# Optimization experiments

Hardware: AMD Instinct MI355X
Metric: run time of the kernel (lower is better)

## Reference

```python
import jax, jax.numpy as jnp
import numpy as np

C = 256      # in/out channels
PSI = 4
W = C // PSI          # window width = 64
D = W // 2            # stride = 32
HEADS = 2 * PSI - 1   # 7


def conv_bn_relu(x, Wmat, scale, bias):
    # 1x1 conv (no bias) + inference-mode BN (folded to per-channel scale/bias) + ReLU
    y = jnp.einsum('oc,bcn->bon', Wmat, x)
    return jax.nn.relu(y * scale[:, None] + bias[:, None])


def setup_inputs() -> dict:
    key = jax.random.key(0)
    ks = jax.random.split(key, 16)
    B, N = 4, 2048
    x = jax.random.normal(ks[0], (B, C, N), dtype=jnp.float32)
    Wq = jax.random.normal(ks[1], (C, C), dtype=jnp.float32) / np.sqrt(C)
    Wk = jax.random.normal(ks[2], (C, C), dtype=jnp.float32) / np.sqrt(C)
    Wv = jax.random.normal(ks[3], (C, C), dtype=jnp.float32) / np.sqrt(C)
    sq = jax.random.uniform(ks[4], (C,), dtype=jnp.float32, minval=0.5, maxval=1.5)
    bq = jax.random.normal(ks[5], (C,), dtype=jnp.float32) * 0.1
    sk = jax.random.uniform(ks[6], (C,), dtype=jnp.float32, minval=0.5, maxval=1.5)
    bk = jax.random.normal(ks[7], (C,), dtype=jnp.float32) * 0.1
    sv = jax.random.uniform(ks[8], (C,), dtype=jnp.float32, minval=0.5, maxval=1.5)
    bv = jax.random.normal(ks[9], (C,), dtype=jnp.float32) * 0.1
    Wf = jax.random.normal(ks[10], (C, HEADS * W), dtype=jnp.float32) / np.sqrt(HEADS * W)
    bf = jax.random.normal(ks[11], (C,), dtype=jnp.float32) * 0.1
    sf = jax.random.uniform(ks[12], (C,), dtype=jnp.float32, minval=0.5, maxval=1.5)
    bff = jax.random.normal(ks[13], (C,), dtype=jnp.float32) * 0.1
    return dict(x=x, Wq=Wq, sq=sq, bq=bq, Wk=Wk, sk=sk, bk=bk,
                Wv=Wv, sv=sv, bv=bv, Wf=Wf, bf=bf, sf=sf, bff=bff)


def reference(x, Wq, sq, bq, Wk, sk, bk, Wv, sv, bv, Wf, bf, sf, bff):
    q = conv_bn_relu(x, Wq, sq, bq)   # [B, C, N]
    k = conv_bn_relu(x, Wk, sk, bk)
    v = conv_bn_relu(x, Wv, sv, bv)

    # overlapping channel windows: head m covers channels [m*D, m*D+W)
    win = jnp.arange(HEADS)[:, None] * D + jnp.arange(W)[None, :]  # [HEADS, W]
    qw = q[:, win, :]  # [B, HEADS, W, N]
    kw = k[:, win, :]
    vw = v[:, win, :]

    # a_m = q_m^T k_m over channel window -> [B, HEADS, N, N]
    attn = jnp.einsum('bhwn,bhwm->bhnm', qw, kw)
    attn = jax.nn.softmax(attn, axis=-1)
    # o_m = (a_m v_m^T)^T -> [B, HEADS, W, N]
    o = jnp.einsum('bhnm,bhwm->bhwn', attn, vw)

    B, _, _, N = o.shape
    O = o.reshape(B, HEADS * W, N)  # concat heads along channel dim

    # fusion: 1x1 conv (with bias) + BN + ReLU
    y = jnp.einsum('oc,bcn->bon', Wf, O) + bf[:, None]
    return jax.nn.relu(y * sf[:, None] + bff[:, None])
```

## Files before the change

kernel.cpp:

```cpp
#include <hip/hip_runtime.h>
#include <hip/hip_bf16.h>

typedef __attribute__((ext_vector_type(8))) short bf16x8;
typedef __attribute__((ext_vector_type(4))) float f32x4;

namespace {
constexpr int kC = 256;
constexpr int kN = 2048;
constexpr int kB = 4;
constexpr int kHeads = 7;
constexpr int kOC = kHeads * 64;
constexpr float kLog2e = 1.44269504f;
}

static __device__ __forceinline__ float bf2f(ushort u) {
    union { unsigned u; float f; } v; v.u = ((unsigned)u) << 16;
    return v.f;
}
static __device__ __forceinline__ unsigned pk_bf16(float a, float b) {
    __hip_bfloat162 h = __float22bfloat162_rn(make_float2(a, b));
    union { __hip_bfloat162 h; unsigned u; } v; v.h = h;
    return v.u;
}
static __device__ __forceinline__ ushort4 pack4bf(float a, float b, float c, float d) {
    union { ushort4 s; uint2 u; } v;
    v.u.x = pk_bf16(a, b); v.u.y = pk_bf16(c, d);
    return v.s;
}
static __device__ __forceinline__ float fexp2(float x) {
#if __has_builtin(__builtin_amdgcn_exp2f)
    return __builtin_amdgcn_exp2f(x);
#else
    return exp2f(x);
#endif
}
static __device__ __forceinline__ void g2l16(const ushort* g, ushort* l) {
    __builtin_amdgcn_global_load_lds(
        (const __attribute__((address_space(1))) void*)g,
        (__attribute__((address_space(3))) void*)l,
        16, 0, 0);
}

__global__ __launch_bounds__(256) void prep_kernel(
    const float* __restrict__ x,
    const float* __restrict__ Wq, const float* __restrict__ Wk,
    const float* __restrict__ Wv, const float* __restrict__ Wf,
    ushort* __restrict__ xT,
    ushort* __restrict__ wq, ushort* __restrict__ wk,
    ushort* __restrict__ wv, ushort* __restrict__ wf)
{
    __shared__ float T[64][65];
    const int bid = blockIdx.x;
    const int tid = threadIdx.x;
    if (bid < 512) {
        const int nt = bid & 31, ct = (bid >> 5) & 3, b = bid >> 7;
        const float* xb = x + ((size_t)b * kC + ct * 64) * kN + nt * 64;
#pragma unroll
        for (int p = 0; p < 16; ++p) {
            int idx = p * 256 + tid;
            int cc = idx >> 6, nn = idx & 63;
            T[cc][nn] = xb[(size_t)cc * kN + nn];
        }
        __syncthreads();
        ushort* xTb = xT + ((size_t)b * kN + nt * 64) * kC + ct * 64;
#pragma unroll
        for (int p = 0; p < 4; ++p) {
            int nn = p * 16 + (tid >> 4);
            int c4 = (tid & 15) * 4;
            *(ushort4*)&xTb[(size_t)nn * kC + c4] =
                pack4bf(T[c4 + 0][nn], T[c4 + 1][nn], T[c4 + 2][nn], T[c4 + 3][nn]);
        }
    } else {
        const int j = bid - 512;
        const int which = j / 112, bx = j % 112;
        const float* src = which == 0 ? Wq : which == 1 ? Wk : which == 2 ? Wv : Wf;
        ushort* dst      = which == 0 ? wq : which == 1 ? wk : which == 2 ? wv : wf;
        int n = (which == 3) ? kC * kOC : kC * kC;
        int i = (bx * 256 + tid) * 4;
        if (i < n) {
            float4 v = *(const float4*)(src + i);
            *(ushort4*)(dst + i) = pack4bf(v.x, v.y, v.z, v.w);
        }
    }
}

__global__ __launch_bounds__(256, 2) void qkv_kernel(
    const ushort* __restrict__ xT,
    const ushort* __restrict__ Wqb, const ushort* __restrict__ Wkb, const ushort* __restrict__ Wvb,
    const float* __restrict__ sq, const float* __restrict__ bq,
    const float* __restrict__ sk, const float* __restrict__ bk,
    const float* __restrict__ sv, const float* __restrict__ bv,
    ushort* __restrict__ qT, ushort* __restrict__ kT, ushort* __restrict__ vB)
{
    const int nt  = blockIdx.x;
    const int ot  = blockIdx.y;
    const int b   = blockIdx.z / 3;
    const int mat = blockIdx.z % 3;
    const ushort* Wb = mat == 0 ? Wqb : mat == 1 ? Wkb : Wvb;
    const float* sm = mat == 0 ? sq : mat == 1 ? sk : sv;
    const float* bm = mat == 0 ? bq : mat == 1 ? bk : bv;

    __shared__ __align__(16) ushort lds[4][128 * 64];

    const int tid = threadIdx.x;
    const int lane = tid & 63, wav = tid >> 6;
    const int quad = lane >> 4, l16 = lane & 15;

    const ushort* xTb = xT + ((size_t)b * kN + nt * 128) * kC;
    const ushort* Wt  = Wb + (size_t)(ot * 128) * kC;

    f32x4 acc[8][2];
#pragma unroll
    for (int mt = 0; mt < 8; ++mt)
#pragma unroll
        for (int ntt = 0; ntt < 2; ++ntt)
#pragma unroll
            for (int r = 0; r < 4; ++r) acc[mt][ntt][r] = 0.f;

    const int sa   = lane >> 3;
    const int sblk = (lane & 7) ^ sa;
    auto dmaK = [&](int k0, int buf) {
#pragma unroll
        for (int p = 0; p < 4; ++p) {
            int row = wav * 32 + p * 8 + sa;
            size_t so = (size_t)row * kC + k0 + sblk * 8;
            int dbase = (wav * 32 + p * 8) * 64;
            g2l16(Wt + so,  &lds[buf][dbase]);
            g2l16(xTb + so, &lds[2 + buf][dbase]);
        }
    };

    dmaK(0, 0);
    __syncthreads();

    for (int kt = 0; kt < 4; ++kt) {
        const int cur = kt & 1;
        const bool more = (kt < 3);
        if (more) dmaK((kt + 1) * 64, cur ^ 1);

        const ushort* rowB = (mat < 2) ? lds[cur] : lds[2 + cur];
        const ushort* colB = (mat < 2) ? lds[2 + cur] : lds[cur];
#pragma unroll
        for (int ks = 0; ks < 2; ++ks) {
            bf16x8 bfr[2];
#pragma unroll
            for (int ntt = 0; ntt < 2; ++ntt) {
                int row = wav * 32 + ntt * 16 + l16;
                bfr[ntt] = *(const bf16x8*)&colB[row * 64 + (((ks * 4 + quad) ^ (row & 7)) * 8)];
            }
#pragma unroll
            for (int mt = 0; mt < 8; ++mt) {
                int row = mt * 16 + l16;
                bf16x8 af = *(const bf16x8*)&rowB[row * 64 + (((ks * 4 + quad) ^ (row & 7)) * 8)];
#pragma unroll
                for (int ntt = 0; ntt < 2; ++ntt)
                    acc[mt][ntt] = __builtin_amdgcn_mfma_f32_16x16x32_bf16(
                        af, bfr[ntt], acc[mt][ntt], 0, 0, 0);
            }
        }
        __syncthreads();
    }

    ushort* sT = &lds[0][0];
    const float qs = (mat == 0) ? kLog2e : 1.f;

    if (mat < 2) {
#pragma unroll
        for (int mt = 0; mt < 8; ++mt) {
            float4 sc4 = *(const float4*)&sm[ot * 128 + mt * 16 + quad * 4];
            float4 bi4 = *(const float4*)&bm[ot * 128 + mt * 16 + quad * 4];
#pragma unroll
            for (int ntt = 0; ntt < 2; ++ntt) {
                int nrow = wav * 32 + ntt * 16 + l16;
                float v0 = fmaf(acc[mt][ntt][0], sc4.x, bi4.x) * qs;
                float v1 = fmaf(acc[mt][ntt][1], sc4.y, bi4.y) * qs;
                float v2 = fmaf(acc[mt][ntt][2], sc4.z, bi4.z) * qs;
                float v3 = fmaf(acc[mt][ntt][3], sc4.w, bi4.w) * qs;
                int cb = (mt * 2 + (quad >> 1)) ^ (nrow & 15);
                *(ushort4*)&sT[nrow * 128 + cb * 8 + (quad & 1) * 4] =
                    pack4bf(v0 > 0.f ? v0 : 0.f, v1 > 0.f ? v1 : 0.f,
                            v2 > 0.f ? v2 : 0.f, v3 > 0.f ? v3 : 0.f);
            }
        }
        __syncthreads();
        ushort* out = (mat == 0) ? qT : kT;
#pragma unroll
        for (int p = 0; p < 8; ++p) {
            int idx = p * 256 + tid;
            int row = idx >> 4, blk = idx & 15;
            int4 d = *(const int4*)&sT[row * 128 + ((blk ^ (row & 15)) * 8)];
            *(int4*)&out[((size_t)b * kN + nt * 128 + row) * kC + ot * 128 + blk * 8] = d;
        }
    } else {
#pragma unroll
        for (int ntt = 0; ntt < 2; ++ntt) {
            int orow = wav * 32 + ntt * 16 + l16;
            float sc = sm[ot * 128 + orow], bi = bm[ot * 128 + orow];
#pragma unroll
            for (int mt = 0; mt < 8; ++mt) {
                float v0 = fmaf(acc[mt][ntt][0], sc, bi);
                float v1 = fmaf(acc[mt][ntt][1], sc, bi);
                float v2 = fmaf(acc[mt][ntt][2], sc, bi);
                float v3 = fmaf(acc[mt][ntt][3], sc, bi);
                int cb = (mt * 2 + (quad >> 1)) ^ (orow & 15);
                *(ushort4*)&sT[orow * 128 + cb * 8 + (quad & 1) * 4] =
                    pack4bf(v0 > 0.f ? v0 : 0.f, v1 > 0.f ? v1 : 0.f,
                            v2 > 0.f ? v2 : 0.f, v3 > 0.f ? v3 : 0.f);
            }
        }
        __syncthreads();
#pragma unroll
        for (int p = 0; p < 8; ++p) {
            int idx = p * 256 + tid;
            int row = idx >> 4, blk = idx & 15;
            int4 d = *(const int4*)&sT[row * 128 + ((blk ^ (row & 15)) * 8)];
            *(int4*)&vB[((size_t)b * kC + ot * 128 + row) * kN + nt * 128 + blk * 8] = d;
        }
    }
}

__global__ __launch_bounds__(512, 2) void attn_kernel(
    const ushort* __restrict__ qT, const ushort* __restrict__ kT,
    const ushort* __restrict__ vB,
    ushort* __restrict__ Opart)
{
    const int j   = blockIdx.x;
    const int lid = (j & 7) * 28 + (j >> 3);
    const int b   = lid / 56;
    const int r2  = lid % 56;
    const int h   = r2 % 7;
    const int nt  = r2 / 7;
    const int n0  = nt * 256;

    const int tid = threadIdx.x;
    const int lane = tid & 63, wav = tid >> 6;
    const int quad = lane >> 4, l16 = lane & 15;

    __shared__ __align__(16) ushort sKV[2][8192];

    const ushort* qTb = qT + (size_t)b * kN * kC;
    const ushort* kTb = kT + (size_t)b * kN * kC;
    const ushort* vbb = vB + ((size_t)b * kC + h * 32) * kN;

    const int arr   = wav >> 2;
    const int rbase = (wav & 3) * 16;

    bf16x8 qf[2][2];
#pragma unroll
    for (int kk = 0; kk < 2; ++kk)
#pragma unroll
        for (int nt2 = 0; nt2 < 2; ++nt2) {
            int ng = n0 + wav * 32 + nt2 * 16 + l16;
            qf[kk][nt2] = *(const bf16x8*)(qTb + (size_t)ng * kC + h * 32 + kk * 32 + quad * 8);
        }

    f32x4 oacc[4][2];
#pragma unroll
    for (int wt = 0; wt < 4; ++wt)
#pragma unroll
        for (int nt2 = 0; nt2 < 2; ++nt2)
#pragma unroll
            for (int r = 0; r < 4; ++r) oacc[wt][nt2][r] = 0.f;
    float li[2] = {0.f, 0.f};

    const int NIT = kN / 64;

    const int sa   = lane >> 3;
    const int sblk = (lane & 7) ^ sa;
    auto dmaTile = [&](int m0, int buf) {
#pragma unroll
        for (int p = 0; p < 2; ++p) {
            int rl = rbase + p * 8 + sa;
            const ushort* src = (arr == 0)
                ? (kTb + (size_t)(m0 + rl) * kC + h * 32 + sblk * 8)
                : (vbb + (size_t)rl * kN + m0 + sblk * 8);
            g2l16(src, &sKV[buf][arr * 4096 + (rbase + p * 8) * 64]);
        }
    };

    dmaTile(0, 0);
    __syncthreads();

    for (int it = 0; it < NIT; ++it) {
        const int cur = it & 1;
        const bool more = (it + 1 < NIT);
        if (more) dmaTile((it + 1) * 64, cur ^ 1);

        const ushort* sK = &sKV[cur][0];
        const ushort* sV = &sKV[cur][4096];

        f32x4 sacc[4][2];
#pragma unroll
        for (int mt = 0; mt < 4; ++mt)
#pragma unroll
            for (int nt2 = 0; nt2 < 2; ++nt2)
#pragma unroll
                for (int r = 0; r < 4; ++r) sacc[mt][nt2][r] = 0.f;
        __builtin_amdgcn_s_setprio(1);
#pragma unroll
        for (int kk = 0; kk < 2; ++kk)
#pragma unroll
            for (int mt = 0; mt < 4; ++mt) {
                int row = mt * 16 + l16;
                bf16x8 af = *(const bf16x8*)&sK[row * 64 + (((kk * 4 + quad) ^ (row & 7)) * 8)];
#pragma unroll
                for (int nt2 = 0; nt2 < 2; ++nt2)
                    sacc[mt][nt2] = __builtin_amdgcn_mfma_f32_16x16x32_bf16(
                        af, qf[kk][nt2], sacc[mt][nt2], 0, 0, 0);
            }
        __builtin_amdgcn_s_setprio(0);

        unsigned d[2][4][2];
#pragma unroll
        for (int nt2 = 0; nt2 < 2; ++nt2) {
            float sum = 0.f;
#pragma unroll
            for (int mt = 0; mt < 4; ++mt) {
                float p0 = fexp2(sacc[mt][nt2][0]);
                float p1 = fexp2(sacc[mt][nt2][1]);
                float p2 = fexp2(sacc[mt][nt2][2]);
                float p3 = fexp2(sacc[mt][nt2][3]);
                sum += (p0 + p1) + (p2 + p3);
                d[nt2][mt][0] = pk_bf16(p0, p1);
                d[nt2][mt][1] = pk_bf16(p2, p3);
            }
            li[nt2] += sum;
        }

#pragma unroll
        for (int ks = 0; ks < 2; ++ks) {
            bf16x8 pf[2];
#pragma unroll
            for (int nt2 = 0; nt2 < 2; ++nt2) {
                union { unsigned w[4]; bf16x8 v8; } pu;
#if __has_builtin(__builtin_amdgcn_permlane32_swap) && __has_builtin(__builtin_amdgcn_permlane16_swap)
#pragma unroll
                for (int rd = 0; rd < 2; ++rd) {
                    unsigned a = d[nt2][2 * ks][rd], bb = d[nt2][2 * ks + 1][rd];
                    auto r32 = __builtin_amdgcn_permlane32_swap(a, bb, false, false);
                    auto r16 = __builtin_amdgcn_permlane16_swap(r32[0], r32[1], false, false);
                    pu.w[rd]     = r16[0];
                    pu.w[2 + rd] = r16[1];
                }
#else
                const int gx = ((lane & 16) << 1) + l16;
                const int gy = gx + 16;
                const bool lo = (lane < 32);
#pragma unroll
                for (int rd = 0; rd < 2; ++rd) {
                    unsigned u = d[nt2][2 * ks][rd], v = d[nt2][2 * ks + 1][rd];
                    unsigned xu = (unsigned)__shfl((int)u, gx);
                    unsigned xv = (unsigned)__shfl((int)v, gx);
                    unsigned yu = (unsigned)__shfl((int)u, gy);
                    unsigned yv = (unsigned)__shfl((int)v, gy);
                    pu.w[rd]     = lo ? xu : xv;
                    pu.w[2 + rd] = lo ? yu : yv;
                }
#endif
                pf[nt2] = pu.v8;
            }
            __builtin_amdgcn_s_setprio(1);
#pragma unroll
            for (int wt = 0; wt < 4; ++wt) {
                int wr = wt * 16 + l16;
                bf16x8 vf = *(const bf16x8*)&sV[wr * 64 + (((ks * 4 + quad) ^ (wr & 7)) * 8)];
#pragma unroll
                for (int nt2 = 0; nt2 < 2; ++nt2)
                    oacc[wt][nt2] = __builtin_amdgcn_mfma_f32_16x16x32_bf16(
                        vf, pf[nt2], oacc[wt][nt2], 0, 0, 0);
            }
            __builtin_amdgcn_s_setprio(0);
        }

        __syncthreads();
    }

#pragma unroll
    for (int nt2 = 0; nt2 < 2; ++nt2) {
        li[nt2] += __shfl_xor(li[nt2], 16);
        li[nt2] += __shfl_xor(li[nt2], 32);
    }
    ushort* sT = &sKV[0][0];
#pragma unroll
    for (int wt = 0; wt < 4; ++wt)
#pragma unroll
        for (int nt2 = 0; nt2 < 2; ++nt2) {
            float inv = 1.f / li[nt2];
            int nrow = wav * 32 + nt2 * 16 + l16;
            int cb = (wt * 2 + (quad >> 1)) ^ (nrow & 7);
            *(ushort4*)&sT[nrow * 64 + cb * 8 + (quad & 1) * 4] =
                pack4bf(oacc[wt][nt2][0] * inv, oacc[wt][nt2][1] * inv,
                        oacc[wt][nt2][2] * inv, oacc[wt][nt2][3] * inv);
        }
    __syncthreads();
    int rsub = tid >> 3, blk = tid & 7;
#pragma unroll
    for (int p = 0; p < 4; ++p) {
        int row = p * 64 + rsub;
        int4 dd = *(const int4*)&sT[row * 64 + ((blk ^ (row & 7)) * 8)];
        *(int4*)&Opart[((size_t)b * kN + n0 + row) * kOC + h * 64 + blk * 8] = dd;
    }
}

__global__ __launch_bounds__(256, 4) void proj_kernel(
    const ushort* __restrict__ Opart, const ushort* __restrict__ Wfb,
    const float* __restrict__ bf_, const float* __restrict__ sf,
    const float* __restrict__ bff, float* __restrict__ out)
{
    const int nt = blockIdx.x;
    const int ot = blockIdx.y;
    const int b  = blockIdx.z;
    __shared__ __align__(16) ushort sA[2][64 * 64];
    __shared__ __align__(16) ushort sB[2][64 * 64];
    const int tid = threadIdx.x;
    const int lane = tid & 63, wav = tid >> 6;
    const int quad = lane >> 4, l16 = lane & 15;

    const ushort* Wt = Wfb + (size_t)(ot * 64) * kOC;
    const ushort* Ob = Opart + ((size_t)b * kN + nt * 64) * kOC;

    f32x4 acc[4];
#pragma unroll
    for (int ntt = 0; ntt < 4; ++ntt)
#pragma unroll
        for (int r = 0; r < 4; ++r) acc[ntt][r] = 0.f;

    const int sa   = lane >> 3;
    const int sblk = (lane & 7) ^ sa;
    auto dmaT = [&](int kt, int buf) {
        int k0 = kt * 64;
#pragma unroll
        for (int p = 0; p < 2; ++p) {
            int row = wav * 16 + p * 8 + sa;
            int dbase = (wav * 16 + p * 8) * 64;
            g2l16(Wt + (size_t)row * kOC + k0 + sblk * 8, &sA[buf][dbase]);
            g2l16(Ob + (size_t)row * kOC + k0 + sblk * 8, &sB[buf][dbase]);
        }
    };

    dmaT(0, 0);
    __syncthreads();

    for (int kt = 0; kt < 7; ++kt) {
        const int cur = kt & 1;
        const bool more = (kt < 6);
        if (more) dmaT(kt + 1, cur ^ 1);
#pragma unroll
        for (int ks = 0; ks < 2; ++ks) {
            int arow = wav * 16 + l16;
            bf16x8 af = *(const bf16x8*)&sA[cur][arow * 64 + (((ks * 4 + quad) ^ (arow & 7)) * 8)];
#pragma unroll
            for (int ntt = 0; ntt < 4; ++ntt) {
                int brow = ntt * 16 + l16;
                bf16x8 bfr = *(const bf16x8*)&sB[cur][brow * 64 + (((ks * 4 + quad) ^ (brow & 7)) * 8)];
                acc[ntt] = __builtin_amdgcn_mfma_f32_16x16x32_bf16(af, bfr, acc[ntt], 0, 0, 0);
            }
        }
        __syncthreads();
    }
#pragma unroll
    for (int r = 0; r < 4; ++r) {
        int o = ot * 64 + wav * 16 + quad * 4 + r;
        float bfv = bf_[o], sfv = sf[o], bffv = bff[o];
#pragma unroll
        for (int ntt = 0; ntt < 4; ++ntt) {
            int n = nt * 64 + ntt * 16 + l16;
            float y = fmaf(acc[ntt][r] + bfv, sfv, bffv);
            out[((size_t)b * kC + o) * kN + n] = y > 0.f ? y : 0.f;
        }
    }
}

extern "C" void kernel_launch(void* const* d_in, const int* in_sizes, int n_in,
                              void* d_out, int out_size, void* d_ws, size_t ws_size,
                              hipStream_t stream) {
    const float* x   = (const float*)d_in[0];
    const float* Wq  = (const float*)d_in[1];
    const float* sq  = (const float*)d_in[2];
    const float* bq  = (const float*)d_in[3];
    const float* Wk  = (const float*)d_in[4];
    const float* sk  = (const float*)d_in[5];
    const float* bk  = (const float*)d_in[6];
    const float* Wv  = (const float*)d_in[7];
    const float* sv  = (const float*)d_in[8];
    const float* bv  = (const float*)d_in[9];
    const float* Wf  = (const float*)d_in[10];
    const float* bf_ = (const float*)d_in[11];
    const float* sf  = (const float*)d_in[12];
    const float* bff = (const float*)d_in[13];
    float* out = (float*)d_out;

    char* ws = (char*)d_ws;
    ushort* xT  = (ushort*)(ws);
    ushort* Wqb = (ushort*)(ws + 4194304);
    ushort* Wkb = (ushort*)(ws + 4325376);
    ushort* Wvb = (ushort*)(ws + 4456448);
    ushort* Wfb = (ushort*)(ws + 4587520);
    ushort* qT  = (ushort*)(ws + 4816896);
    ushort* kT  = (ushort*)(ws + 9011200);
    ushort* vB  = (ushort*)(ws + 13205504);
    ushort* Opart = (ushort*)(ws + 17399808);

    prep_kernel<<<dim3(960), 256, 0, stream>>>(
        x, Wq, Wk, Wv, Wf, xT, Wqb, Wkb, Wvb, Wfb);
    qkv_kernel<<<dim3(kN / 128, kC / 128, kB * 3), 256, 0, stream>>>(
        xT, Wqb, Wkb, Wvb, sq, bq, sk, bk, sv, bv, qT, kT, vB);
    attn_kernel<<<dim3(224), 512, 0, stream>>>(
        qT, kT, vB, Opart);
    proj_kernel<<<dim3(kN / 64, kC / 64, kB), 256, 0, stream>>>(
        Opart, Wfb, bf_, sf, bff, out);
}
```

Baseline: 153.2 us.

## Split QKV GEMM tile across 8 waves and remap blocks across XCDs

The QKV projection kernel now runs 512 threads per block instead of 256. Each wave computes a 64x32 sub-tile instead of 128x32, halving per-wave accumulators and adding latency hiding. The 3D grid is flattened to 384 blocks with a remapping that groups consecutive logical tiles onto the same XCD, intended to improve L2 reuse of x and weights. The extra waves share the same LDS buffers and barriers, so synchronisation cost per block rises.

```diff
diff --git a/kernel.cpp b/kernel.cpp
--- a/kernel.cpp
+++ b/kernel.cpp
@@ -84,7 +84,7 @@
     }
 }
 
-__global__ __launch_bounds__(256, 2) void qkv_kernel(
+__global__ __launch_bounds__(512, 2) void qkv_kernel(
     const ushort* __restrict__ xT,
     const ushort* __restrict__ Wqb, const ushort* __restrict__ Wkb, const ushort* __restrict__ Wvb,
     const float* __restrict__ sq, const float* __restrict__ bq,
@@ -92,10 +92,13 @@
     const float* __restrict__ sv, const float* __restrict__ bv,
     ushort* __restrict__ qT, ushort* __restrict__ kT, ushort* __restrict__ vB)
 {
-    const int nt  = blockIdx.x;
-    const int ot  = blockIdx.y;
-    const int b   = blockIdx.z / 3;
-    const int mat = blockIdx.z % 3;
+    const int j   = blockIdx.x;
+    const int lid = (j & 7) * 48 + (j >> 3);
+    const int nt  = lid & 15;
+    const int ot  = (lid >> 4) & 1;
+    const int zz  = lid >> 5;
+    const int b   = zz / 3;
+    const int mat = zz % 3;
     const ushort* Wb = mat == 0 ? Wqb : mat == 1 ? Wkb : Wvb;
     const float* sm = mat == 0 ? sq : mat == 1 ? sk : sv;
     const float* bm = mat == 0 ? bq : mat == 1 ? bk : bv;
@@ -105,13 +108,15 @@
     const int tid = threadIdx.x;
     const int lane = tid & 63, wav = tid >> 6;
     const int quad = lane >> 4, l16 = lane & 15;
+    const int oh = wav >> 2;
+    const int nq = wav & 3;
 
     const ushort* xTb = xT + ((size_t)b * kN + nt * 128) * kC;
     const ushort* Wt  = Wb + (size_t)(ot * 128) * kC;
 
-    f32x4 acc[8][2];
-#pragma unroll
-    for (int mt = 0; mt < 8; ++mt)
+    f32x4 acc[4][2];
+#pragma unroll
+    for (int mt = 0; mt < 4; ++mt)
 #pragma unroll
         for (int ntt = 0; ntt < 2; ++ntt)
 #pragma unroll
@@ -121,10 +126,10 @@
     const int sblk = (lane & 7) ^ sa;
     auto dmaK = [&](int k0, int buf) {
 #pragma unroll
-        for (int p = 0; p < 4; ++p) {
-            int row = wav * 32 + p * 8 + sa;
+        for (int p = 0; p < 2; ++p) {
+            int row = wav * 16 + p * 8 + sa;
             size_t so = (size_t)row * kC + k0 + sblk * 8;
-            int dbase = (wav * 32 + p * 8) * 64;
+            int dbase = (wav * 16 + p * 8) * 64;
             g2l16(Wt + so,  &lds[buf][dbase]);
             g2l16(xTb + so, &lds[2 + buf][dbase]);
         }
@@ -145,12 +150,12 @@
             bf16x8 bfr[2];
 #pragma unroll
             for (int ntt = 0; ntt < 2; ++ntt) {
-                int row = wav * 32 + ntt * 16 + l16;
+                int row = nq * 32 + ntt * 16 + l16;
                 bfr[ntt] = *(const bf16x8*)&colB[row * 64 + (((ks * 4 + quad) ^ (row & 7)) * 8)];
             }
 #pragma unroll
-            for (int mt = 0; mt < 8; ++mt) {
-                int row = mt * 16 + l16;
+            for (int mt = 0; mt < 4; ++mt) {
+                int row = oh * 64 + mt * 16 + l16;
                 bf16x8 af = *(const bf16x8*)&rowB[row * 64 + (((ks * 4 + quad) ^ (row & 7)) * 8)];
 #pragma unroll
                 for (int ntt = 0; ntt < 2; ++ntt)
@@ -166,17 +171,17 @@
 
     if (mat < 2) {
 #pragma unroll
-        for (int mt = 0; mt < 8; ++mt) {
-            float4 sc4 = *(const float4*)&sm[ot * 128 + mt * 16 + quad * 4];
-            float4 bi4 = *(const float4*)&bm[ot * 128 + mt * 16 + quad * 4];
+        for (int mt = 0; mt < 4; ++mt) {
+            float4 sc4 = *(const float4*)&sm[ot * 128 + oh * 64 + mt * 16 + quad * 4];
+            float4 bi4 = *(const float4*)&bm[ot * 128 + oh * 64 + mt * 16 + quad * 4];
 #pragma unroll
             for (int ntt = 0; ntt < 2; ++ntt) {
-                int nrow = wav * 32 + ntt * 16 + l16;
+                int nrow = nq * 32 + ntt * 16 + l16;
                 float v0 = fmaf(acc[mt][ntt][0], sc4.x, bi4.x) * qs;
                 float v1 = fmaf(acc[mt][ntt][1], sc4.y, bi4.y) * qs;
                 float v2 = fmaf(acc[mt][ntt][2], sc4.z, bi4.z) * qs;
                 float v3 = fmaf(acc[mt][ntt][3], sc4.w, bi4.w) * qs;
-                int cb = (mt * 2 + (quad >> 1)) ^ (nrow & 15);
+                int cb = (oh * 8 + mt * 2 + (quad >> 1)) ^ (nrow & 15);
                 *(ushort4*)&sT[nrow * 128 + cb * 8 + (quad & 1) * 4] =
                     pack4bf(v0 > 0.f ? v0 : 0.f, v1 > 0.f ? v1 : 0.f,
                             v2 > 0.f ? v2 : 0.f, v3 > 0.f ? v3 : 0.f);
@@ -185,8 +190,8 @@
         __syncthreads();
         ushort* out = (mat == 0) ? qT : kT;
 #pragma unroll
-        for (int p = 0; p < 8; ++p) {
-            int idx = p * 256 + tid;
+        for (int p = 0; p < 4; ++p) {
+            int idx = p * 512 + tid;
             int row = idx >> 4, blk = idx & 15;
             int4 d = *(const int4*)&sT[row * 128 + ((blk ^ (row & 15)) * 8)];
             *(int4*)&out[((size_t)b * kN + nt * 128 + row) * kC + ot * 128 + blk * 8] = d;
@@ -194,15 +199,15 @@
     } else {
 #pragma unroll
         for (int ntt = 0; ntt < 2; ++ntt) {
-            int orow = wav * 32 + ntt * 16 + l16;
+            int orow = nq * 32 + ntt * 16 + l16;
             float sc = sm[ot * 128 + orow], bi = bm[ot * 128 + orow];
 #pragma unroll
-            for (int mt = 0; mt < 8; ++mt) {
+            for (int mt = 0; mt < 4; ++mt) {
                 float v0 = fmaf(acc[mt][ntt][0], sc, bi);
                 float v1 = fmaf(acc[mt][ntt][1], sc, bi);
                 float v2 = fmaf(acc[mt][ntt][2], sc, bi);
                 float v3 = fmaf(acc[mt][ntt][3], sc, bi);
-                int cb = (mt * 2 + (quad >> 1)) ^ (orow & 15);
+                int cb = (oh * 8 + mt * 2 + (quad >> 1)) ^ (orow & 15);
                 *(ushort4*)&sT[orow * 128 + cb * 8 + (quad & 1) * 4] =
                     pack4bf(v0 > 0.f ? v0 : 0.f, v1 > 0.f ? v1 : 0.f,
                             v2 > 0.f ? v2 : 0.f, v3 > 0.f ? v3 : 0.f);
@@ -210,8 +215,8 @@
         }
         __syncthreads();
 #pragma unroll
-        for (int p = 0; p < 8; ++p) {
-            int idx = p * 256 + tid;
+        for (int p = 0; p < 4; ++p) {
+            int idx = p * 512 + tid;
             int row = idx >> 4, blk = idx & 15;
             int4 d = *(const int4*)&sT[row * 128 + ((blk ^ (row & 15)) * 8)];
             *(int4*)&vB[((size_t)b * kC + ot * 128 + row) * kN + nt * 128 + blk * 8] = d;
@@ -503,7 +508,7 @@
 
     prep_kernel<<<dim3(960), 256, 0, stream>>>(
         x, Wq, Wk, Wv, Wf, xT, Wqb, Wkb, Wvb, Wfb);
-    qkv_kernel<<<dim3(kN / 128, kC / 128, kB * 3), 256, 0, stream>>>(
+    qkv_kernel<<<dim3(384), 512, 0, stream>>>(
         xT, Wqb, Wkb, Wvb, sq, bq, sk, bk, sv, bv, qT, kT, vB);
     attn_kernel<<<dim3(224), 512, 0, stream>>>(
         qT, kT, vB, Opart);
```

Result: no change. 151.1 us, median of 2 (-1.3%).
